# Performance work log

Measured on AMD Instinct MI355X. Metric: run time of the kernel, lower is better.

The kernel has to match this reference:

```python
import jax, jax.numpy as jnp
import numpy as np

EMBED_DIM = 128
TEMP_DIM = EMBED_DIM // 4  # 32
NUM_TYPES = 50
DATE_SCALE = 1825.0
LN_EPS = 1e-5


def _layernorm(x, w, b):
    m = jnp.mean(x, axis=-1, keepdims=True)
    v = jnp.mean((x - m) ** 2, axis=-1, keepdims=True)
    return (x - m) * jax.lax.rsqrt(v + LN_EPS) * w + b


def setup_inputs() -> dict:
    key = jax.random.key(0)
    ks = jax.random.split(key, 16)
    B, L = 4096, 200
    inp = {
        "treatment_ids": jax.random.randint(ks[0], (B, L), 0, NUM_TYPES, dtype=jnp.int64 if jax.config.jax_enable_x64 else jnp.int32),
        "dates": jax.random.uniform(ks[1], (B, L), dtype=jnp.float32) * DATE_SCALE,
        "lengths": jax.random.randint(ks[2], (B,), 0, L + 1, dtype=jnp.int32),
        # parameters
        "emb": jax.random.normal(ks[3], (NUM_TYPES, EMBED_DIM), jnp.float32),
        "tp_w": jax.random.normal(ks[4], (1, TEMP_DIM), jnp.float32) * 0.1,
        "tp_b": jnp.zeros((TEMP_DIM,), jnp.float32),
        "tp_lnw": jnp.ones((TEMP_DIM,), jnp.float32),
        "tp_lnb": jnp.zeros((TEMP_DIM,), jnp.float32),
        "w1": jax.random.normal(ks[5], (EMBED_DIM + TEMP_DIM, EMBED_DIM), jnp.float32) * 0.05,
        "b1": jnp.zeros((EMBED_DIM,), jnp.float32),
        "ln1w": jnp.ones((EMBED_DIM,), jnp.float32),
        "ln1b": jnp.zeros((EMBED_DIM,), jnp.float32),
        "w2": jax.random.normal(ks[6], (EMBED_DIM, EMBED_DIM), jnp.float32) * 0.05,
        "b2": jnp.zeros((EMBED_DIM,), jnp.float32),
        "ln2w": jnp.ones((EMBED_DIM,), jnp.float32),
        "ln2b": jnp.zeros((EMBED_DIM,), jnp.float32),
    }
    return inp


def reference(treatment_ids, dates, lengths, emb, tp_w, tp_b, tp_lnw, tp_lnb,
              w1, b1, ln1w, ln1b, w2, b2, ln2w, ln2b):
    B, L = treatment_ids.shape
    mask = (jnp.arange(L)[None, :] < lengths[:, None]).astype(dates.dtype)  # [B, L]

    # embedding lookup [B, L, D]
    treat = emb[treatment_ids]

    # temporal projection: Linear(1 -> D/4) + LN + GELU
    dn = (dates / DATE_SCALE)[..., None]                      # [B, L, 1]
    temporal = dn * tp_w[0] + tp_b                            # [B, L, D/4]
    temporal = jax.nn.gelu(_layernorm(temporal, tp_lnw, tp_lnb), approximate=False)

    combined = jnp.concatenate([treat, temporal], axis=-1)    # [B, L, D + D/4]

    # sequence encoder (dropout is identity at eval)
    h = jnp.einsum("blk,kd->bld", combined, w1) + b1
    h = jax.nn.gelu(_layernorm(h, ln1w, ln1b), approximate=False)
    h = jnp.einsum("blk,kd->bld", h, w2) + b2
    h = _layernorm(h, ln2w, ln2b)                             # [B, L, D]

    # masked mean pool; empty histories -> zeros
    counts = jnp.sum(mask, axis=1, keepdims=True)             # [B, 1]
    pooled = jnp.sum(h * mask[..., None], axis=1) / jnp.maximum(counts, 1.0)
    return jnp.where(counts > 0, pooled, 0.0)                 # [B, D]
```

## Files before the change

kernel.cpp:

```cpp
#include <hip/hip_runtime.h>
#include <cmath>

#define LN_EPS 1e-5f

typedef float  f32x4  __attribute__((ext_vector_type(4)));
typedef short  short8 __attribute__((ext_vector_type(8)));
typedef unsigned int uint4v __attribute__((ext_vector_type(4)));

#define W1TF_U4 512
#define W2F_U4  2048
#define E1_U4   1650
#define WLDS_U4 2560

__device__ __forceinline__ unsigned short f32_bf16_rne(float f) {
    union { float f; unsigned u; } v; v.f = f;
    unsigned r = v.u + 0x7FFFu + ((v.u >> 16) & 1u);
    return (unsigned short)(r >> 16);
}

__device__ __forceinline__ unsigned cvt_pk_bf16(float lo, float hi) {
    unsigned r;
    asm("v_cvt_pk_bf16_f32 %0, %1, %2" : "=v"(r) : "v"(lo), "v"(hi));
    return r;
}

__device__ __forceinline__ float gelu_f(float x) {
    float ax = fabsf(x);
    float a  = ax * 0.70710678118654752f;
    float t  = __builtin_amdgcn_rcpf(fmaf(0.3275911f, a, 1.0f));
    float p  = t * fmaf(t, fmaf(t, fmaf(t, fmaf(t, 1.061405429f, -1.453152027f),
                                        1.421413741f), -0.284496736f), 0.254829592f);
    float e  = __builtin_amdgcn_exp2f(-1.44269504089f * a * a);
    float E  = fmaf(-p, e, 1.0f);
    return 0.5f * fmaf(ax, E, x);
}

template<int C>
__device__ __forceinline__ float dpp_radd(float x) {
    int t = __builtin_amdgcn_update_dpp(0, __builtin_bit_cast(int, x), C, 0xF, 0xF, true);
    return x + __builtin_bit_cast(float, t);
}
__device__ __forceinline__ float red16(float x) {
    x = dpp_radd<0x128>(x);
    x = dpp_radd<0x124>(x);
    x = dpp_radd<0x122>(x);
    x = dpp_radd<0x121>(x);
    return x;
}

__global__ void prep_kernel(const float* __restrict__ w1, const float* __restrict__ w2,
                            const float* __restrict__ emb,
                            const float* __restrict__ tp_w, const float* __restrict__ tp_b,
                            unsigned* __restrict__ ws) {
    const int tid = blockIdx.x * 256 + threadIdx.x;
    uint4v* w1tf = (uint4v*)ws;
    uint4v* w2f  = w1tf + W1TF_U4;
    float*  E1   = (float*)(w2f + W2F_U4);
    float*  tps  = E1 + 6600;

    for (int i = tid; i < W1TF_U4; i += 8192) {
        const int lane = i & 63, nt = i >> 6;
        const int k0 = 128 + (lane >> 4) * 8, n = nt * 16 + (lane & 15);
        uint4v r;
        #pragma unroll
        for (int j2 = 0; j2 < 4; ++j2) {
            unsigned lo = f32_bf16_rne(w1[(k0 + 2 * j2) * 128 + n]);
            unsigned hi = f32_bf16_rne(w1[(k0 + 2 * j2 + 1) * 128 + n]);
            r[j2] = lo | (hi << 16);
        }
        w1tf[i] = r;
    }
    for (int i = tid; i < W2F_U4; i += 8192) {
        const int lane = i & 63, nt = (i >> 6) & 7, kt = i >> 9;
        const int k0 = kt * 32 + (lane >> 4) * 8, n = nt * 16 + (lane & 15);
        uint4v r;
        #pragma unroll
        for (int j2 = 0; j2 < 4; ++j2) {
            unsigned lo = f32_bf16_rne(w2[(k0 + 2 * j2) * 128 + n]);
            unsigned hi = f32_bf16_rne(w2[(k0 + 2 * j2 + 1) * 128 + n]);
            r[j2] = lo | (hi << 16);
        }
        w2f[i] = r;
    }
    if (tid < 6400) {
        const int t = tid >> 7, n = tid & 127;
        float s = 0.f;
        for (int k = 0; k < 128; ++k)
            s = fmaf(emb[t * 128 + k], w1[k * 128 + n], s);
        E1[t * 132 + n] = s;
    }
    if (tid == 0) {
        float Sw = 0.f, Sb = 0.f, Sww = 0.f, Swb = 0.f, Sbb = 0.f;
        for (int j = 0; j < 32; ++j) {
            const float ww = tp_w[j], bb = tp_b[j];
            Sw += ww; Sb += bb; Sww += ww * ww; Swb += ww * bb; Sbb += bb * bb;
        }
        tps[0] = Sw; tps[1] = Sb; tps[2] = Sww; tps[3] = Swb; tps[4] = Sbb;
    }
}

__global__ __launch_bounds__(768, 3) void encoder_mfma(
    const int*   __restrict__ tids,  const float* __restrict__ dates,
    const int*   __restrict__ lengths,
    const float* __restrict__ tp_w,  const float* __restrict__ tp_b,
    const float* __restrict__ tp_lnw,const float* __restrict__ tp_lnb,
    const float* __restrict__ b1,    const float* __restrict__ ln1w, const float* __restrict__ ln1b,
    const float* __restrict__ b2,    const float* __restrict__ ln2w, const float* __restrict__ ln2b,
    const unsigned* __restrict__ ws, float* __restrict__ out,
    int B, int L)
{
    __shared__ __align__(16) uint4v wlds[WLDS_U4];
    __shared__ __align__(16) float  E1lds[6600];
    __shared__ __align__(16) unsigned short a2[12][4][64][8];
    __shared__ float poolbuf[3][4][128];
    __shared__ __align__(16) f32x4 tcoef[32];
    __shared__ __align__(16) f32x4 ecoef1[128];
    __shared__ __align__(16) f32x4 ecoef2[128];

    const int tid = threadIdx.x;
    const int lane = tid & 63, w = tid >> 6;
    const int c = lane & 15, g = lane >> 4;
    const int row = w >> 2, wr = w & 3;
    const int b   = blockIdx.x * 3 + row;

    for (int i = tid; i < WLDS_U4; i += 768)
        wlds[i] = ((const uint4v*)ws)[i];
    for (int i = tid; i < E1_U4; i += 768)
        ((uint4v*)E1lds)[i] = ((const uint4v*)ws)[WLDS_U4 + i];

    const float* tps = (const float*)((const uint4v*)ws + WLDS_U4 + E1_U4);

    if (tid < 32)  tcoef[tid]  = (f32x4){tp_w[tid], tp_b[tid], tp_lnw[tid], tp_lnb[tid]};
    if (tid < 128) {
        ecoef1[tid] = (f32x4){b1[tid], ln1w[tid], ln1b[tid], 0.f};
        ecoef2[tid] = (f32x4){b2[tid], ln2w[tid], ln2b[tid], 0.f};
    }
    __syncthreads();

    const float Sw = tps[0], Sb = tps[1], Sww = tps[2], Swb = tps[3], Sbb = tps[4];

    const int len = (b < B) ? min(max(lengths[b], 0), L) : 0;
    const int ntiles = (len + 15) >> 4;

    float pool[8];
    #pragma unroll
    for (int nt = 0; nt < 8; ++nt) pool[nt] = 0.f;
    const int srl = lane ^ ((lane >> 3) & 3);

    for (int t = wr; t < ntiles; t += 4) {
        const int R0 = t << 4;
        const int pc = min(R0 + c, L - 1);
        const float d = dates[b * L + pc] * (1.f / 1825.f);
        int idr[4];
        #pragma unroll
        for (int r = 0; r < 4; ++r)
            idr[r] = tids[b * L + min(R0 + 4 * g + r, L - 1)];

        short8 tfrag;
        {
            const float tm = fmaf(d, Sw, Sb) * (1.f / 32.f);
            float tv = fmaf(d * d, Sww, fmaf(2.f * d, Swb, Sbb)) * (1.f / 32.f) - tm * tm;
            const float trs = rsqrtf(fmaxf(tv, 0.f) + LN_EPS);
            const int j0 = g * 8;
            uint4v r;
            #pragma unroll
            for (int j2 = 0; j2 < 4; ++j2) {
                const f32x4 t0 = tcoef[j0 + 2*j2];
                const f32x4 t1 = tcoef[j0 + 2*j2 + 1];
                const float y0 = fmaf((fmaf(d, t0[0], t0[1]) - tm) * trs, t0[2], t0[3]);
                const float y1 = fmaf((fmaf(d, t1[0], t1[1]) - tm) * trs, t1[2], t1[3]);
                r[j2] = cvt_pk_bf16(gelu_f(y0), gelu_f(y1));
            }
            union { uint4v u; short8 s; } cv; cv.u = r;
            tfrag = cv.s;
        }

        f32x4 acc[8];
        #pragma unroll
        for (int r = 0; r < 4; ++r) {
            const int e1base = idr[r] * 132 + c;
            #pragma unroll
            for (int nt = 0; nt < 8; ++nt)
                acc[nt][r] = E1lds[e1base + nt * 16];
        }
        __builtin_amdgcn_s_setprio(1);
        #pragma unroll
        for (int nt = 0; nt < 8; ++nt) {
            const short8 bf = ((const short8*)wlds)[nt * 64 + lane];
            acc[nt] = __builtin_amdgcn_mfma_f32_16x16x32_bf16(tfrag, bf, acc[nt], 0, 0, 0);
        }
        __builtin_amdgcn_s_setprio(0);

        {
            f32x4 e1[8];
            #pragma unroll
            for (int nt = 0; nt < 8; ++nt) e1[nt] = ecoef1[nt * 16 + c];
            #pragma unroll
            for (int r = 0; r < 4; ++r) {
                float v[8], s = 0.f, q = 0.f;
                #pragma unroll
                for (int nt = 0; nt < 8; ++nt) {
                    v[nt] = acc[nt][r] + e1[nt][0];
                    s += v[nt]; q = fmaf(v[nt], v[nt], q);
                }
                s = red16(s); q = red16(q);
                const float mean = s * (1.f / 128.f);
                const float var  = fmaxf(q * (1.f / 128.f) - mean * mean, 0.f);
                const float rstd = rsqrtf(var + LN_EPS);
                const int mrow = 4 * g + r;
                #pragma unroll
                for (int n2 = 0; n2 < 4; ++n2) {
                    const float y0 = gelu_f(fmaf((v[2*n2]   - mean) * rstd, e1[2*n2][1],   e1[2*n2][2]));
                    const float y1 = gelu_f(fmaf((v[2*n2+1] - mean) * rstd, e1[2*n2+1][1], e1[2*n2+1][2]));
                    const unsigned pk = cvt_pk_bf16(y0, y1);
                    {
                        const int kcol  = (2*n2) * 16 + c;
                        const int row64 = ((kcol >> 3) & 3) * 16 + mrow;
                        const int srow  = row64 ^ ((row64 >> 3) & 3);
                        a2[w][kcol >> 5][srow][kcol & 7] = (unsigned short)(pk & 0xffffu);
                    }
                    {
                        const int kcol  = (2*n2+1) * 16 + c;
                        const int row64 = ((kcol >> 3) & 3) * 16 + mrow;
                        const int srow  = row64 ^ ((row64 >> 3) & 3);
                        a2[w][kcol >> 5][srow][kcol & 7] = (unsigned short)(pk >> 16);
                    }
                }
            }
        }

        asm volatile("" ::: "memory");

        f32x4 acc2[8];
        #pragma unroll
        for (int nt = 0; nt < 8; ++nt) acc2[nt] = (f32x4){0.f, 0.f, 0.f, 0.f};
        __builtin_amdgcn_s_setprio(1);
        #pragma unroll
        for (int kt2 = 0; kt2 < 4; ++kt2) {
            short8 af;
            __builtin_memcpy(&af, &a2[w][kt2][srl][0], 16);
            #pragma unroll
            for (int nt = 0; nt < 8; ++nt) {
                const short8 bf = ((const short8*)(wlds + W1TF_U4))[(kt2 * 8 + nt) * 64 + lane];
                acc2[nt] = __builtin_amdgcn_mfma_f32_16x16x32_bf16(af, bf, acc2[nt], 0, 0, 0);
            }
        }
        __builtin_amdgcn_s_setprio(0);

        asm volatile("" ::: "memory");

        {
            f32x4 e2[8];
            #pragma unroll
            for (int nt = 0; nt < 8; ++nt) e2[nt] = ecoef2[nt * 16 + c];
            #pragma unroll
            for (int r = 0; r < 4; ++r) {
                float v[8], s = 0.f, q = 0.f;
                #pragma unroll
                for (int nt = 0; nt < 8; ++nt) {
                    v[nt] = acc2[nt][r] + e2[nt][0];
                    s += v[nt]; q = fmaf(v[nt], v[nt], q);
                }
                s = red16(s); q = red16(q);
                const float mean = s * (1.f / 128.f);
                const float var  = fmaxf(q * (1.f / 128.f) - mean * mean, 0.f);
                const float rstd = rsqrtf(var + LN_EPS);
                const float msk = ((R0 + 4 * g + r) < len) ? 1.f : 0.f;
                #pragma unroll
                for (int nt = 0; nt < 8; ++nt) {
                    const float y = fmaf((v[nt] - mean) * rstd, e2[nt][1], e2[nt][2]);
                    pool[nt] = fmaf(y, msk, pool[nt]);
                }
            }
        }
    }

    #pragma unroll
    for (int nt = 0; nt < 8; ++nt) {
        float tv = pool[nt];
        tv += __shfl_xor(tv, 16);
        tv += __shfl_xor(tv, 32);
        pool[nt] = tv;
    }
    if (g == 0) {
        #pragma unroll
        for (int nt = 0; nt < 8; ++nt) poolbuf[row][wr][nt * 16 + c] = pool[nt];
    }
    __syncthreads();
    if (tid < 384) {
        const int r3  = tid >> 7;
        const int col = tid & 127;
        const int bo  = blockIdx.x * 3 + r3;
        if (bo < B) {
            const int len2 = min(max(lengths[bo], 0), L);
            const float s = poolbuf[r3][0][col] + poolbuf[r3][1][col]
                          + poolbuf[r3][2][col] + poolbuf[r3][3][col];
            out[bo * 128 + col] = (len2 > 0) ? s / (float)len2 : 0.f;
        }
    }
}

extern "C" void kernel_launch(void* const* d_in, const int* in_sizes, int n_in,
                              void* d_out, int out_size, void* d_ws, size_t ws_size,
                              hipStream_t stream) {
    const int*   tids    = (const int*)  d_in[0];
    const float* dates   = (const float*)d_in[1];
    const int*   lengths = (const int*)  d_in[2];
    const float* emb     = (const float*)d_in[3];
    const float* tp_w    = (const float*)d_in[4];
    const float* tp_b    = (const float*)d_in[5];
    const float* tp_lnw  = (const float*)d_in[6];
    const float* tp_lnb  = (const float*)d_in[7];
    const float* w1      = (const float*)d_in[8];
    const float* b1      = (const float*)d_in[9];
    const float* ln1w    = (const float*)d_in[10];
    const float* ln1b    = (const float*)d_in[11];
    const float* w2      = (const float*)d_in[12];
    const float* b2      = (const float*)d_in[13];
    const float* ln2w    = (const float*)d_in[14];
    const float* ln2b    = (const float*)d_in[15];
    float* out = (float*)d_out;

    const int B = in_sizes[2];
    const int L = in_sizes[0] / B;

    hipLaunchKernelGGL(prep_kernel, dim3(32), dim3(256), 0, stream,
                       w1, w2, emb, tp_w, tp_b, (unsigned*)d_ws);
    hipLaunchKernelGGL(encoder_mfma, dim3((B + 2) / 3), dim3(768), 0, stream,
                       tids, dates, lengths, tp_w, tp_b, tp_lnw, tp_lnb,
                       b1, ln1w, ln1b, b2, ln2w, ln2b,
                       (const unsigned*)d_ws, out, B, L);
}
```

Baseline: 211.5 us.

## Balance row tiles across all 12 waves of a block instead of per-row waves

Previously each of the 3 batch rows in a block was owned by 4 fixed waves, so waves for short sequences sat idle while others processed long ones. The tiles of all three rows are now concatenated and striped over all 12 waves, with per-row pooling accumulators and a 12-way reduction in shared memory. This costs extra registers for three pool arrays, a branchy row lookup per tile and a larger poolbuf, which may pressure the 3-blocks-per-CU occupancy target. The setup kernel's embedding-times-W1 loop also gets an unroll pragma.

```diff
diff --git a/kernel.cpp b/kernel.cpp
--- a/kernel.cpp
+++ b/kernel.cpp
@@ -85,6 +85,7 @@
     if (tid < 6400) {
         const int t = tid >> 7, n = tid & 127;
         float s = 0.f;
+        #pragma unroll 4
         for (int k = 0; k < 128; ++k)
             s = fmaf(emb[t * 128 + k], w1[k * 128 + n], s);
         E1[t * 132 + n] = s;
@@ -112,7 +113,7 @@
     __shared__ __align__(16) uint4v wlds[WLDS_U4];
     __shared__ __align__(16) float  E1lds[6600];
     __shared__ __align__(16) unsigned short a2[12][4][64][8];
-    __shared__ float poolbuf[3][4][128];
+    __shared__ float poolbuf[3][12][128];
     __shared__ __align__(16) f32x4 tcoef[32];
     __shared__ __align__(16) f32x4 ecoef1[128];
     __shared__ __align__(16) f32x4 ecoef2[128];
@@ -120,8 +121,7 @@
     const int tid = threadIdx.x;
     const int lane = tid & 63, w = tid >> 6;
     const int c = lane & 15, g = lane >> 4;
-    const int row = w >> 2, wr = w & 3;
-    const int b   = blockIdx.x * 3 + row;
+    const int b0 = blockIdx.x * 3;
 
     for (int i = tid; i < WLDS_U4; i += 768)
         wlds[i] = ((const uint4v*)ws)[i];
@@ -139,22 +139,31 @@
 
     const float Sw = tps[0], Sb = tps[1], Sww = tps[2], Swb = tps[3], Sbb = tps[4];
 
-    const int len = (b < B) ? min(max(lengths[b], 0), L) : 0;
-    const int ntiles = (len + 15) >> 4;
-
-    float pool[8];
+    const int len0 = (b0 + 0 < B) ? min(max(lengths[b0 + 0], 0), L) : 0;
+    const int len1 = (b0 + 1 < B) ? min(max(lengths[b0 + 1], 0), L) : 0;
+    const int len2 = (b0 + 2 < B) ? min(max(lengths[b0 + 2], 0), L) : 0;
+    const int nt0 = (len0 + 15) >> 4, nt1 = (len1 + 15) >> 4, nt2 = (len2 + 15) >> 4;
+    const int cum1 = nt0, cum2 = nt0 + nt1, T = cum2 + nt2;
+
+    float pool0[8], pool1[8], pool2[8];
     #pragma unroll
-    for (int nt = 0; nt < 8; ++nt) pool[nt] = 0.f;
+    for (int nt = 0; nt < 8; ++nt) { pool0[nt] = 0.f; pool1[nt] = 0.f; pool2[nt] = 0.f; }
     const int srl = lane ^ ((lane >> 3) & 3);
 
-    for (int t = wr; t < ntiles; t += 4) {
-        const int R0 = t << 4;
+    for (int t = w; t < T; t += 12) {
+        const int row  = (t >= cum2) ? 2 : ((t >= cum1) ? 1 : 0);
+        const int tl   = t - ((row == 2) ? cum2 : ((row == 1) ? cum1 : 0));
+        const int bb   = b0 + row;
+        const int lenr = (row == 2) ? len2 : ((row == 1) ? len1 : len0);
+        const int R0   = tl << 4;
+        const long base = (long)bb * L;
+
         const int pc = min(R0 + c, L - 1);
-        const float d = dates[b * L + pc] * (1.f / 1825.f);
+        const float d = dates[base + pc] * (1.f / 1825.f);
         int idr[4];
         #pragma unroll
         for (int r = 0; r < 4; ++r)
-            idr[r] = tids[b * L + min(R0 + 4 * g + r, L - 1)];
+            idr[r] = tids[base + min(R0 + 4 * g + r, L - 1)];
 
         short8 tfrag;
         {
@@ -253,6 +262,9 @@
             f32x4 e2[8];
             #pragma unroll
             for (int nt = 0; nt < 8; ++nt) e2[nt] = ecoef2[nt * 16 + c];
+            float ptile[8];
+            #pragma unroll
+            for (int nt = 0; nt < 8; ++nt) ptile[nt] = 0.f;
             #pragma unroll
             for (int r = 0; r < 4; ++r) {
                 float v[8], s = 0.f, q = 0.f;
@@ -265,37 +277,51 @@
                 const float mean = s * (1.f / 128.f);
                 const float var  = fmaxf(q * (1.f / 128.f) - mean * mean, 0.f);
                 const float rstd = rsqrtf(var + LN_EPS);
-                const float msk = ((R0 + 4 * g + r) < len) ? 1.f : 0.f;
+                const float msk = ((R0 + 4 * g + r) < lenr) ? 1.f : 0.f;
                 #pragma unroll
                 for (int nt = 0; nt < 8; ++nt) {
                     const float y = fmaf((v[nt] - mean) * rstd, e2[nt][1], e2[nt][2]);
-                    pool[nt] = fmaf(y, msk, pool[nt]);
+                    ptile[nt] = fmaf(y, msk, ptile[nt]);
                 }
+            }
+            if (row == 0) {
+                #pragma unroll
+                for (int nt = 0; nt < 8; ++nt) pool0[nt] += ptile[nt];
+            } else if (row == 1) {
+                #pragma unroll
+                for (int nt = 0; nt < 8; ++nt) pool1[nt] += ptile[nt];
+            } else {
+                #pragma unroll
+                for (int nt = 0; nt < 8; ++nt) pool2[nt] += ptile[nt];
             }
         }
     }
 
     #pragma unroll
     for (int nt = 0; nt < 8; ++nt) {
-        float tv = pool[nt];
-        tv += __shfl_xor(tv, 16);
-        tv += __shfl_xor(tv, 32);
-        pool[nt] = tv;
+        float t0 = pool0[nt]; t0 += __shfl_xor(t0, 16); t0 += __shfl_xor(t0, 32); pool0[nt] = t0;
+        float t1 = pool1[nt]; t1 += __shfl_xor(t1, 16); t1 += __shfl_xor(t1, 32); pool1[nt] = t1;
+        float t2 = pool2[nt]; t2 += __shfl_xor(t2, 16); t2 += __shfl_xor(t2, 32); pool2[nt] = t2;
     }
     if (g == 0) {
         #pragma unroll
-        for (int nt = 0; nt < 8; ++nt) poolbuf[row][wr][nt * 16 + c] = pool[nt];
+        for (int nt = 0; nt < 8; ++nt) {
+            poolbuf[0][w][nt * 16 + c] = pool0[nt];
+            poolbuf[1][w][nt * 16 + c] = pool1[nt];
+            poolbuf[2][w][nt * 16 + c] = pool2[nt];
+        }
     }
     __syncthreads();
     if (tid < 384) {
         const int r3  = tid >> 7;
         const int col = tid & 127;
-        const int bo  = blockIdx.x * 3 + r3;
+        const int bo  = b0 + r3;
         if (bo < B) {
-            const int len2 = min(max(lengths[bo], 0), L);
-            const float s = poolbuf[r3][0][col] + poolbuf[r3][1][col]
-                          + poolbuf[r3][2][col] + poolbuf[r3][3][col];
-            out[bo * 128 + col] = (len2 > 0) ? s / (float)len2 : 0.f;
+            const int lenb = min(max(lengths[bo], 0), L);
+            float s = 0.f;
+            #pragma unroll
+            for (int k = 0; k < 12; ++k) s += poolbuf[r3][k][col];
+            out[bo * 128 + col] = (lenb > 0) ? s / (float)lenb : 0.f;
         }
     }
 }
```

New measurement: 208.3 us. Within noise of the previous version (-1.5%).

## Load-balance tiles across 16 waves over 4 rows with LDS atomic pooling

Applied to the files above, without the earlier changes.

Blocks grow from 768 to 1024 threads and now cover 4 batch rows instead of 3. The 16-row tiles of all four rows go into one flat list that is strided across all 16 waves, which removes the imbalance from variable sequence lengths under the fixed 4-waves-per-row split. Each wave reduces its per-tile partial pool and adds it to a shared per-row buffer with LDS atomicAdd, replacing the per-wave buffer and final sum. The risks are lower occupancy from launch_bounds(1024,4) and the added LDS atomic and reduction cost per tile. A small unroll pragma is also added to the prep kernel.

```diff
diff --git a/kernel.cpp b/kernel.cpp
--- a/kernel.cpp
+++ b/kernel.cpp
@@ -85,6 +85,7 @@
     if (tid < 6400) {
         const int t = tid >> 7, n = tid & 127;
         float s = 0.f;
+        #pragma unroll 4
         for (int k = 0; k < 128; ++k)
             s = fmaf(emb[t * 128 + k], w1[k * 128 + n], s);
         E1[t * 132 + n] = s;
@@ -99,7 +100,7 @@
     }
 }
 
-__global__ __launch_bounds__(768, 3) void encoder_mfma(
+__global__ __launch_bounds__(1024, 4) void encoder_mfma(
     const int*   __restrict__ tids,  const float* __restrict__ dates,
     const int*   __restrict__ lengths,
     const float* __restrict__ tp_w,  const float* __restrict__ tp_b,
@@ -111,8 +112,8 @@
 {
     __shared__ __align__(16) uint4v wlds[WLDS_U4];
     __shared__ __align__(16) float  E1lds[6600];
-    __shared__ __align__(16) unsigned short a2[12][4][64][8];
-    __shared__ float poolbuf[3][4][128];
+    __shared__ __align__(16) unsigned short a2[16][4][64][8];
+    __shared__ float poolrow[4][128];
     __shared__ __align__(16) f32x4 tcoef[32];
     __shared__ __align__(16) f32x4 ecoef1[128];
     __shared__ __align__(16) f32x4 ecoef2[128];
@@ -120,13 +121,13 @@
     const int tid = threadIdx.x;
     const int lane = tid & 63, w = tid >> 6;
     const int c = lane & 15, g = lane >> 4;
-    const int row = w >> 2, wr = w & 3;
-    const int b   = blockIdx.x * 3 + row;
-
-    for (int i = tid; i < WLDS_U4; i += 768)
+    const int b0 = blockIdx.x * 4;
+
+    for (int i = tid; i < WLDS_U4; i += 1024)
         wlds[i] = ((const uint4v*)ws)[i];
-    for (int i = tid; i < E1_U4; i += 768)
+    for (int i = tid; i < E1_U4; i += 1024)
         ((uint4v*)E1lds)[i] = ((const uint4v*)ws)[WLDS_U4 + i];
+    if (tid < 512) poolrow[tid >> 7][tid & 127] = 0.f;
 
     const float* tps = (const float*)((const uint4v*)ws + WLDS_U4 + E1_U4);
 
@@ -139,22 +140,31 @@
 
     const float Sw = tps[0], Sb = tps[1], Sww = tps[2], Swb = tps[3], Sbb = tps[4];
 
-    const int len = (b < B) ? min(max(lengths[b], 0), L) : 0;
-    const int ntiles = (len + 15) >> 4;
-
-    float pool[8];
-    #pragma unroll
-    for (int nt = 0; nt < 8; ++nt) pool[nt] = 0.f;
+    const int len0 = (b0 + 0 < B) ? min(max(lengths[b0 + 0], 0), L) : 0;
+    const int len1 = (b0 + 1 < B) ? min(max(lengths[b0 + 1], 0), L) : 0;
+    const int len2 = (b0 + 2 < B) ? min(max(lengths[b0 + 2], 0), L) : 0;
+    const int len3 = (b0 + 3 < B) ? min(max(lengths[b0 + 3], 0), L) : 0;
+    const int nt0 = (len0 + 15) >> 4, nt1 = (len1 + 15) >> 4;
+    const int nt2 = (len2 + 15) >> 4, nt3 = (len3 + 15) >> 4;
+    const int cum1 = nt0, cum2 = nt0 + nt1, cum3 = cum2 + nt2, T = cum3 + nt3;
+
     const int srl = lane ^ ((lane >> 3) & 3);
 
-    for (int t = wr; t < ntiles; t += 4) {
-        const int R0 = t << 4;
+    for (int t = w; t < T; t += 16) {
+        int row, tl, lenr;
+        if (t >= cum3)      { row = 3; tl = t - cum3; lenr = len3; }
+        else if (t >= cum2) { row = 2; tl = t - cum2; lenr = len2; }
+        else if (t >= cum1) { row = 1; tl = t - cum1; lenr = len1; }
+        else                { row = 0; tl = t;        lenr = len0; }
+        const int R0 = tl << 4;
+        const long base = (long)(b0 + row) * L;
+
         const int pc = min(R0 + c, L - 1);
-        const float d = dates[b * L + pc] * (1.f / 1825.f);
+        const float d = dates[base + pc] * (1.f / 1825.f);
         int idr[4];
         #pragma unroll
         for (int r = 0; r < 4; ++r)
-            idr[r] = tids[b * L + min(R0 + 4 * g + r, L - 1)];
+            idr[r] = tids[base + min(R0 + 4 * g + r, L - 1)];
 
         short8 tfrag;
         {
@@ -253,6 +263,9 @@
             f32x4 e2[8];
             #pragma unroll
             for (int nt = 0; nt < 8; ++nt) e2[nt] = ecoef2[nt * 16 + c];
+            float ptile[8];
+            #pragma unroll
+            for (int nt = 0; nt < 8; ++nt) ptile[nt] = 0.f;
             #pragma unroll
             for (int r = 0; r < 4; ++r) {
                 float v[8], s = 0.f, q = 0.f;
@@ -265,37 +278,36 @@
                 const float mean = s * (1.f / 128.f);
                 const float var  = fmaxf(q * (1.f / 128.f) - mean * mean, 0.f);
                 const float rstd = rsqrtf(var + LN_EPS);
-                const float msk = ((R0 + 4 * g + r) < len) ? 1.f : 0.f;
+                const float msk = ((R0 + 4 * g + r) < lenr) ? 1.f : 0.f;
                 #pragma unroll
                 for (int nt = 0; nt < 8; ++nt) {
                     const float y = fmaf((v[nt] - mean) * rstd, e2[nt][1], e2[nt][2]);
-                    pool[nt] = fmaf(y, msk, pool[nt]);
+                    ptile[nt] = fmaf(y, msk, ptile[nt]);
                 }
             }
-        }
-    }
-
-    #pragma unroll
-    for (int nt = 0; nt < 8; ++nt) {
-        float tv = pool[nt];
-        tv += __shfl_xor(tv, 16);
-        tv += __shfl_xor(tv, 32);
-        pool[nt] = tv;
-    }
-    if (g == 0) {
-        #pragma unroll
-        for (int nt = 0; nt < 8; ++nt) poolbuf[row][wr][nt * 16 + c] = pool[nt];
-    }
+            #pragma unroll
+            for (int nt = 0; nt < 8; ++nt) {
+                float tv = ptile[nt];
+                tv += __shfl_xor(tv, 16);
+                tv += __shfl_xor(tv, 32);
+                ptile[nt] = tv;
+            }
+            if (g == 0) {
+                #pragma unroll
+                for (int nt = 0; nt < 8; ++nt)
+                    atomicAdd(&poolrow[row][nt * 16 + c], ptile[nt]);
+            }
+        }
+    }
+
     __syncthreads();
-    if (tid < 384) {
-        const int r3  = tid >> 7;
+    if (tid < 512) {
+        const int r4  = tid >> 7;
         const int col = tid & 127;
-        const int bo  = blockIdx.x * 3 + r3;
+        const int bo  = b0 + r4;
         if (bo < B) {
-            const int len2 = min(max(lengths[bo], 0), L);
-            const float s = poolbuf[r3][0][col] + poolbuf[r3][1][col]
-                          + poolbuf[r3][2][col] + poolbuf[r3][3][col];
-            out[bo * 128 + col] = (len2 > 0) ? s / (float)len2 : 0.f;
+            const int lenb = min(max(lengths[bo], 0), L);
+            out[bo * 128 + col] = (lenb > 0) ? poolrow[r4][col] / (float)lenb : 0.f;
         }
     }
 }
@@ -326,7 +338,7 @@
 
     hipLaunchKernelGGL(prep_kernel, dim3(32), dim3(256), 0, stream,
                        w1, w2, emb, tp_w, tp_b, (unsigned*)d_ws);
-    hipLaunchKernelGGL(encoder_mfma, dim3((B + 2) / 3), dim3(768), 0, stream,
+    hipLaunchKernelGGL(encoder_mfma, dim3((B + 3) / 4), dim3(1024), 0, stream,
                        tids, dates, lengths, tp_w, tp_b, tp_lnw, tp_lnb,
                        b1, ln1w, ln1b, b2, ln2w, ln2b,
                        (const unsigned*)d_ws, out, B, L);
```

New measurement: 217.0 us. +2.6%, slower.
